# Performance work log

Measured on AMD Instinct MI355X. Metric: run time of the kernel, lower is better.

Reference implementation:

```python
import jax, jax.numpy as jnp
import numpy as np

N, E = 30000, 240000          # nodes, edges per view
IN, D, OUT = 512, 128, 64      # in_dim, hidden_dim, out_dim
V, BLK, H, DM = 2, 2, 2, 64    # num_view, blk_size, num_heads, gate max-pool dim
NEG_ATT, NEG_OUT = 0.2, 0.01   # leaky_relu slopes (attention / outer)


def setup_inputs() -> dict:
    key = jax.random.key(0)
    ks = jax.random.split(key, 12)
    s = 0.05
    f32 = jnp.float32
    return {
        "ft": jax.random.normal(ks[0], (N, IN), f32),
        "src": jax.random.randint(ks[1], (V, E), 0, N, jnp.int32),
        "dst": jax.random.randint(ks[2], (V, E), 0, N, jnp.int32),
        "W_proj": jax.random.normal(ks[3], (IN, D), f32) * s,
        "W_embed": jax.random.normal(ks[4], (D, D), f32) * s,
        "a_l": jax.random.normal(ks[5], (V, BLK, H, D), f32) * s,
        "a_r": jax.random.normal(ks[6], (V, BLK, H, D), f32) * s,
        "Wv": jax.random.normal(ks[7], (V, BLK, H, D, D), f32) * s,
        "Wgm": jax.random.normal(ks[8], (V, BLK, D, DM), f32) * s,
        "Wgate": jax.random.normal(ks[9], (V, BLK, 2 * D + DM, H), f32) * s,
        "b_gate": jnp.zeros((V, BLK, H), f32),
        "W_tran": jax.random.normal(ks[10], (2 * D + DM and (D + V * H * D), OUT), f32) * s if False else jax.random.normal(ks[10], (D + V * H * D, OUT), f32) * s,
        "b_tran": jnp.zeros((OUT,), f32),
    }


def _seg_sum(x, idx):
    return jax.ops.segment_sum(x, idx, num_segments=N)


def _cgaan_layer(v, z, s_idx, d_idx, al, ar, wv, wgm, wgate, bg, merge):
    # v: [N,D] values, z: [N,D] attention features ('proj_z')
    # Multi-head attention logits: e_ij = leaky_relu(a_l.z_src + a_r.z_dst)  [E,H]
    logit_l = jnp.einsum("nd,hd->nh", z, al)
    logit_r = jnp.einsum("nd,hd->nh", z, ar)
    e = jax.nn.leaky_relu(logit_l[s_idx] + logit_r[d_idx], NEG_ATT)
    # edge softmax over incoming edges of each dst node
    m = jax.ops.segment_max(e, d_idx, num_segments=N)          # [N,H]
    ex = jnp.exp(e - m[d_idx])
    denom = _seg_sum(ex, d_idx)                                 # [N,H]
    alpha = ex / denom[d_idx]                                   # [E,H]
    # per-head value projection and weighted aggregation
    wvn = jnp.einsum("nd,hde->nhe", v, wv)                      # [N,H,D]
    agg = _seg_sum(alpha[:, :, None] * wvn[s_idx], d_idx)       # [N,H,D]
    # GaAN-style gate: sigmoid(FC([x_i, mean_j v_j, max_j (v_j Wgm)])) -> per-head scalar
    deg = _seg_sum(jnp.ones((s_idx.shape[0],), v.dtype), d_idx)  # [N]
    mean_n = _seg_sum(v[s_idx], d_idx) / jnp.maximum(deg, 1.0)[:, None]
    mx = jax.ops.segment_max((v @ wgm)[s_idx], d_idx, num_segments=N)
    mx = jnp.where(deg[:, None] > 0, mx, 0.0)                   # isolated nodes -> 0
    g = jax.nn.sigmoid(jnp.concatenate([v, mean_n, mx], -1) @ wgate + bg)  # [N,H]
    agg = g[:, :, None] * agg
    if merge == "mean":
        return agg.mean(axis=1)                                 # [N,D]
    return agg.reshape(agg.shape[0], -1)                        # cat -> [N,H*D]


def reference(ft, src, dst, W_proj, W_embed, a_l, a_r, Wv, Wgm, Wgate, b_gate, W_tran, b_tran):
    proj = ft @ W_proj                                          # [N,D]
    cur = [proj for _ in range(V)]
    for i in range(BLK):
        merge = "mean" if i < BLK - 1 else "cat"
        nxt = []
        for j in range(V):
            z = cur[j] @ W_embed
            h = _cgaan_layer(cur[j], z, src[j], dst[j], a_l[j, i], a_r[j, i],
                             Wv[j, i], Wgm[j, i], Wgate[j, i], b_gate[j, i], merge)
            nxt.append(jax.nn.leaky_relu(h, NEG_OUT))
        cur = nxt
    h = jnp.concatenate([proj] + cur, axis=-1)                  # [N, D+V*H*D]
    return h @ W_tran + b_tran
```

## Files before the change

### kernel.cpp

```cpp
#include <hip/hip_runtime.h>
#include <hip/hip_bf16.h>
#include <math.h>

#define NN 30000
#define EE 240000
#define IN_DIM 512
#define DD 128
#define OUTD 64
#define NV 2
#define NBLK 2
#define NH 2
#define DMM 64
#define NEG_ATT 0.2f
#define NEG_OUT 0.01f
#define CH 1024
#define NCH ((NN + CH - 1) / CH)

typedef __attribute__((ext_vector_type(8))) short bf16x8;
typedef __attribute__((ext_vector_type(4))) float f32x4;
typedef __attribute__((ext_vector_type(4))) unsigned short us4;
typedef __attribute__((ext_vector_type(8))) unsigned short us8;

#define OFF_PROJVM 0
#define OFF_WV     131072
#define OFF_WGM    262144
#define OFF_TRAN   278528
#define WT_TOTAL   319488

__device__ __forceinline__ unsigned split_bf(float x) {
  unsigned u = __float_as_uint(x);
  unsigned hb = (u + 0x7FFFu + ((u >> 16) & 1u)) >> 16;
  float hf = __uint_as_float(hb << 16);
  float lo = x - hf;
  unsigned ul = __float_as_uint(lo);
  unsigned lb = (ul + 0x7FFFu + ((ul >> 16) & 1u)) >> 16;
  return hb | (lb << 16);
}

__device__ __forceinline__ unsigned short f2bf(float x) {
  unsigned u = __float_as_uint(x);
  return (unsigned short)((u + 0x7FFFu + ((u >> 16) & 1u)) >> 16);
}
__device__ __forceinline__ float bf2f(unsigned short u) {
  return __uint_as_float((unsigned)u << 16);
}

__device__ __forceinline__ void gload16(void* lds, const void* g) {
  __builtin_amdgcn_global_load_lds((const __attribute__((address_space(1))) unsigned int*)g,
                                   (__attribute__((address_space(3))) unsigned int*)lds, 16, 0, 0);
}

__global__ __launch_bounds__(256) void k_deg(const int* __restrict__ dst, int* __restrict__ deg) {
  int e = blockIdx.x * 256 + threadIdx.x;
  if (e < NV * EE) atomicAdd(&deg[(e / EE) * NN + dst[e]], 1);
}

__global__ __launch_bounds__(256) void k_scan1(const int* __restrict__ deg, int* __restrict__ partial) {
  int b = blockIdx.x, view = b / NCH, ch = b % NCH;
  const int* d = deg + view * NN + ch * CH;
  int rem = min(CH, NN - ch * CH);
  int t = threadIdx.x;
  int s = 0;
  for (int i = t; i < rem; i += 256) s += d[i];
  for (int k = 32; k; k >>= 1) s += __shfl_xor(s, k);
  __shared__ int wsum[4];
  if ((t & 63) == 0) wsum[t >> 6] = s;
  __syncthreads();
  if (t == 0) partial[b] = wsum[0] + wsum[1] + wsum[2] + wsum[3];
}

__global__ void k_scan2(const int* __restrict__ partial, int* __restrict__ chunkoff, int* __restrict__ off) {
  if (threadIdx.x == 0 && blockIdx.x == 0) {
    for (int v = 0; v < NV; v++) {
      int acc = 0;
      for (int c = 0; c < NCH; c++) { chunkoff[v * NCH + c] = acc; acc += partial[v * NCH + c]; }
      off[v * (NN + 1) + NN] = acc;
    }
  }
}

__global__ __launch_bounds__(256) void k_scan3(const int* __restrict__ deg, const int* __restrict__ chunkoff,
                                               int* __restrict__ off) {
  int b = blockIdx.x, view = b / NCH, ch = b % NCH;
  int base = ch * CH;
  const int* d = deg + view * NN;
  int* o = off + view * (NN + 1);
  int t = threadIdx.x, lane = t & 63, w = t >> 6;
  int i0 = base + t * 4;
  int x0 = 0, x1 = 0, x2 = 0, x3 = 0;
  if (i0 + 3 < NN) { int4 q = *(const int4*)(d + i0); x0 = q.x; x1 = q.y; x2 = q.z; x3 = q.w; }
  else {
    if (i0     < NN) x0 = d[i0];
    if (i0 + 1 < NN) x1 = d[i0 + 1];
    if (i0 + 2 < NN) x2 = d[i0 + 2];
  }
  int tot = x0 + x1 + x2 + x3;
  int incl = tot;
  for (int k = 1; k < 64; k <<= 1) { int y = __shfl_up(incl, k); if (lane >= k) incl += y; }
  __shared__ int wt[4];
  if (lane == 63) wt[w] = incl;
  __syncthreads();
  int wexcl = 0;
  for (int k = 0; k < w; k++) wexcl += wt[k];
  int excl = chunkoff[b] + wexcl + incl - tot;
  if (i0     < NN) o[i0]     = excl;
  if (i0 + 1 < NN) o[i0 + 1] = excl + x0;
  if (i0 + 2 < NN) o[i0 + 2] = excl + x0 + x1;
  if (i0 + 3 < NN) o[i0 + 3] = excl + x0 + x1 + x2;
}

__global__ __launch_bounds__(256) void k_fill(const int* __restrict__ src, const int* __restrict__ dst,
                                              const int* __restrict__ off, int* __restrict__ cursor,
                                              int* __restrict__ csr_src) {
  int e = blockIdx.x * 256 + threadIdx.x;
  if (e >= NV * EE) return;
  int view = e / EE;
  int d = dst[e];
  int p = atomicAdd(&cursor[view * NN + d], 1);
  csr_src[view * EE + off[view * (NN + 1) + d] + p] = src[e];
}

__global__ __launch_bounds__(256) void k_prep(const float* __restrict__ W_embed, const float* __restrict__ a_l,
                                              const float* __restrict__ a_r, float* __restrict__ Bl,
                                              float* __restrict__ Br) {
  int idx = blockIdx.x * 256 + threadIdx.x;
  if (idx >= NV * NBLK * DD * NH) return;
  int h = idx & 1, dd = (idx >> 1) & 127, lv = idx >> 8;
  const float* w = W_embed + dd * DD;
  const float* al = a_l + (lv * NH + h) * DD;
  const float* ar = a_r + (lv * NH + h) * DD;
  float sl = 0.f, sr = 0.f;
  for (int e = 0; e < DD; e++) { float we = w[e]; sl += we * al[e]; sr += we * ar[e]; }
  Bl[idx] = sl; Br[idx] = sr;
}

__global__ __launch_bounds__(256) void k_prep2(const float* __restrict__ Wp, const float* __restrict__ Wgm,
                                               float* __restrict__ wf) {
  int idx = blockIdx.x * 256 + threadIdx.x;
  int j = idx >> 15, k = (idx >> 6) & 511, n = idx & 63;
  const float* wp = Wp + (size_t)k * DD;
  const float* wg = Wgm + (size_t)(j * NBLK + 0) * DD * DMM + n;
  float s = 0.f;
  for (int e = 0; e < DD; e++) s += wp[e] * wg[(size_t)e * DMM];
  wf[idx] = s;
}

__global__ __launch_bounds__(256) void k_wsplit(const float* __restrict__ Wp, const float* __restrict__ wf,
                                                const float* __restrict__ Wv, const float* __restrict__ Wgm,
                                                const float* __restrict__ Wt,
                                                unsigned short* __restrict__ hi, unsigned short* __restrict__ lo) {
  int y = blockIdx.y;
  const float* src; int K, N; size_t doff;
  if (y == 0)      { src = Wp;                      K = 512; N = 128; doff = OFF_PROJVM; }
  else if (y <= 2) { int j = y - 1; src = wf + (size_t)j * 512 * 64; K = 512; N = 64; doff = OFF_PROJVM + (size_t)(128 + j * 64) * 512; }
  else if (y <= 6) { int lv = y - 3; src = Wv + (size_t)lv * 32768;  K = 256; N = 128; doff = OFF_WV + (size_t)lv * 32768; }
  else if (y <= 8) { int j = y - 7; src = Wgm + (size_t)(j * NBLK + 1) * 8192; K = 128; N = 64; doff = OFF_WGM + (size_t)j * 8192; }
  else             { src = Wt;                      K = 640; N = 64;  doff = OFF_TRAN; }
  int idx = blockIdx.x * 256 + threadIdx.x;
  if (idx >= K * N) return;
  int n = idx / K, k = idx % K;
  int tk = k >> 6, g = (k >> 3) & 7, j2 = k & 7;
  int ks = (tk << 6) | ((g ^ (n & 7)) << 3) | j2;
  unsigned p = split_bf(src[(size_t)k * N + n]);
  hi[doff + (size_t)n * K + ks] = (unsigned short)(p & 0xFFFFu);
  lo[doff + (size_t)n * K + ks] = (unsigned short)(p >> 16);
}

__global__ __launch_bounds__(256) void k_llr(const unsigned short* __restrict__ p0,
                                             const unsigned short* __restrict__ p1, int ps,
                                             const float* __restrict__ Bl0, const float* __restrict__ Br0,
                                             const float* __restrict__ Bl1, const float* __restrict__ Br1,
                                             float* __restrict__ ll, float* __restrict__ lr) {
  int lane = threadIdx.x & 63, wid = threadIdx.x >> 6;
  int n = blockIdx.x * 4 + wid;
  int k = lane * 2;
  unsigned a = *(const unsigned*)(p0 + (size_t)n * ps + k);
  unsigned b = *(const unsigned*)(p1 + (size_t)n * ps + k);
  float ax = bf2f((unsigned short)a), ay = bf2f((unsigned short)(a >> 16));
  float bx = bf2f((unsigned short)b), by = bf2f((unsigned short)(b >> 16));
  float r[8];
  r[0] = ax * Bl0[k * 2]     + ay * Bl0[k * 2 + 2];
  r[1] = ax * Bl0[k * 2 + 1] + ay * Bl0[k * 2 + 3];
  r[2] = ax * Br0[k * 2]     + ay * Br0[k * 2 + 2];
  r[3] = ax * Br0[k * 2 + 1] + ay * Br0[k * 2 + 3];
  r[4] = bx * Bl1[k * 2]     + by * Bl1[k * 2 + 2];
  r[5] = bx * Bl1[k * 2 + 1] + by * Bl1[k * 2 + 3];
  r[6] = bx * Br1[k * 2]     + by * Br1[k * 2 + 2];
  r[7] = bx * Br1[k * 2 + 1] + by * Br1[k * 2 + 3];
  for (int s = 32; s; s >>= 1)
#pragma unroll
    for (int q = 0; q < 8; q++) r[q] += __shfl_xor(r[q], s);
  if (lane == 0) {
    ll[n * 2] = r[0]; ll[n * 2 + 1] = r[1];
    lr[n * 2] = r[2]; lr[n * 2 + 1] = r[3];
    ll[NN * 2 + n * 2] = r[4]; ll[NN * 2 + n * 2 + 1] = r[5];
    lr[NN * 2 + n * 2] = r[6]; lr[NN * 2 + n * 2 + 1] = r[7];
  }
}

__global__ __launch_bounds__(256) void k_edge(const int* __restrict__ off_, const int* __restrict__ csr_,
                                              const float* __restrict__ ll_, const float* __restrict__ lr_,
                                              const unsigned short* __restrict__ pk_, long viewStride,
                                              int ps, int vmoff0, int vmstep,
                                              const float* __restrict__ Wg_, const float* __restrict__ bg_,
                                              unsigned short* __restrict__ S_) {
  int view = blockIdx.y;
  const int* off = off_ + view * (NN + 1);
  const int* csr = csr_ + (size_t)view * EE;
  const float* ll = ll_ + (size_t)view * NN * 2;
  const float* lr = lr_ + (size_t)view * NN * 2;
  const unsigned short* pk = pk_ + (size_t)view * viewStride;
  int vmoff = vmoff0 + view * vmstep;
  const float* Wg = Wg_ + (size_t)view * NBLK * (2 * DD + DMM) * NH;
  const float* bg = bg_ + view * NBLK * NH;
  unsigned short* S = S_ + (size_t)view * NN * 256;

  int lane = threadIdx.x & 63, wid = threadIdx.x >> 6;
  int n = blockIdx.x * 4 + wid;
  int e0 = off[n], nb = off[n + 1] - e0;
  int half = lane >> 5, hl = lane & 31;
  if (nb == 0) {
    us4 z4 = {0, 0, 0, 0};
    *(us4*)(S + (size_t)n * 256 + half * 128 + 4 * hl) = z4;
    return;
  }
  float lr0 = lr[n * 2], lr1 = lr[n * 2 + 1];
  float sa0[4] = {0.f, 0.f, 0.f, 0.f}, sa1[4] = {0.f, 0.f, 0.f, 0.f}, vs[4] = {0.f, 0.f, 0.f, 0.f};
  float d0 = 0.f, d1 = 0.f, vm0 = -INFINITY, vm1 = -INFINITY;
  for (int base = 0; base < nb; base += 64) {
    int i = base + lane;
    float w0 = 0.f, w1 = 0.f, fv = 0.f; int sidx = 0;
    if (i < nb) {
      sidx = csr[e0 + i];
      float x0 = ll[sidx * 2] + lr0, x1 = ll[sidx * 2 + 1] + lr1;
      x0 = (x0 > 0.f) ? x0 : NEG_ATT * x0;
      x1 = (x1 > 0.f) ? x1 : NEG_ATT * x1;
      w0 = __expf(x0); w1 = __expf(x1); fv = 1.f;
    }
    d0 += w0; d1 += w1;
    int cnt = min(64, nb - base);
    for (int s = 0; 2 * s < cnt; s++) {
      int j = 2 * s + half;
      int se = __shfl(sidx, j);
      float we0 = __shfl(w0, j), we1 = __shfl(w1, j), fe = __shfl(fv, j);
      if (fe != 0.f) {
        const unsigned short* rowp = pk + (size_t)se * ps;
        us4 vq = *(const us4*)(rowp + 4 * hl);
        float v0 = bf2f(vq[0]), v1 = bf2f(vq[1]), v2 = bf2f(vq[2]), v3 = bf2f(vq[3]);
        sa0[0] += we0 * v0; sa0[1] += we0 * v1; sa0[2] += we0 * v2; sa0[3] += we0 * v3;
        sa1[0] += we1 * v0; sa1[1] += we1 * v1; sa1[2] += we1 * v2; sa1[3] += we1 * v3;
        vs[0] += v0; vs[1] += v1; vs[2] += v2; vs[3] += v3;
        unsigned vmu = *(const unsigned*)(rowp + vmoff + 2 * hl);
        vm0 = fmaxf(vm0, bf2f((unsigned short)vmu));
        vm1 = fmaxf(vm1, bf2f((unsigned short)(vmu >> 16)));
      }
    }
  }
#pragma unroll
  for (int k = 0; k < 4; k++) {
    sa0[k] += __shfl_xor(sa0[k], 32);
    sa1[k] += __shfl_xor(sa1[k], 32);
    vs[k]  += __shfl_xor(vs[k], 32);
  }
  vm0 = fmaxf(vm0, __shfl_xor(vm0, 32));
  vm1 = fmaxf(vm1, __shfl_xor(vm1, 32));
  for (int s = 32; s; s >>= 1) { d0 += __shfl_xor(d0, s); d1 += __shfl_xor(d1, s); }
  unsigned vnu = *(const unsigned*)(pk + (size_t)n * ps + 2 * lane);
  float vnx = bf2f((unsigned short)vnu), vny = bf2f((unsigned short)(vnu >> 16));
  float im = 1.f / (float)nb;
  float p0 = vnx * Wg[(2 * lane) * 2]     + vny * Wg[(2 * lane + 1) * 2];
  float p1 = vnx * Wg[(2 * lane) * 2 + 1] + vny * Wg[(2 * lane + 1) * 2 + 1];
  if (half == 0) {
#pragma unroll
    for (int k = 0; k < 4; k++) {
      float mk = vs[k] * im;
      p0 += mk * Wg[(128 + 4 * hl + k) * 2];
      p1 += mk * Wg[(128 + 4 * hl + k) * 2 + 1];
    }
  } else {
    p0 += vm0 * Wg[(256 + 2 * hl) * 2]     + vm1 * Wg[(256 + 2 * hl + 1) * 2];
    p1 += vm0 * Wg[(256 + 2 * hl) * 2 + 1] + vm1 * Wg[(256 + 2 * hl + 1) * 2 + 1];
  }
  for (int s = 32; s; s >>= 1) { p0 += __shfl_xor(p0, s); p1 += __shfl_xor(p1, s); }
  float g0 = 1.f / (1.f + __expf(-(p0 + bg[0])));
  float g1 = 1.f / (1.f + __expf(-(p1 + bg[1])));
  float q0 = g0 / d0, q1 = g1 / d1;
  us4 o4;
  if (half == 0) {
    o4[0] = f2bf(sa0[0] * q0); o4[1] = f2bf(sa0[1] * q0);
    o4[2] = f2bf(sa0[2] * q0); o4[3] = f2bf(sa0[3] * q0);
  } else {
    o4[0] = f2bf(sa1[0] * q1); o4[1] = f2bf(sa1[1] * q1);
    o4[2] = f2bf(sa1[2] * q1); o4[3] = f2bf(sa1[3] * q1);
  }
  *(us4*)(S + (size_t)n * 256 + half * 128 + 4 * hl) = o4;
}

struct GB {
  const void* A[4];
  unsigned long long bofs[4];
  float* C[4];
  unsigned short* P[4];
  int ldc[4];
  int pldc[4];
};

template <int BN, bool ABF>
__global__ __launch_bounds__(256) void gemm_mfma(
    GB gb, const unsigned short* __restrict__ Bth, const unsigned short* __restrict__ Btl,
    int lda, int ldb, int M, int K,
    const float* __restrict__ bias, float fs, int flags) {
  constexpr int NSUB = BN / 32;
  constexpr int CPW = BN / 32;
  __shared__ __align__(16) unsigned short Ah[64][64];
  __shared__ __align__(16) unsigned short Al[ABF ? 2 : 64][64];
  __shared__ __align__(16) unsigned short Bh[BN][64], Bl[BN][64];
  const int z = blockIdx.z;
  const float* __restrict__ Af = (const float*)gb.A[z];
  const unsigned short* __restrict__ Ab = (const unsigned short*)gb.A[z];
  float* __restrict__ C = gb.C[z];
  unsigned short* __restrict__ P = gb.P[z];
  const int ldc = gb.ldc[z], pldc = gb.pldc[z];
  const size_t bofs = gb.bofs[z];
  const int t = threadIdx.x;
  const int lane = t & 63, wv = t >> 6;
  const int lm = lane & 15, lg = lane >> 4;
  const int m0w = (wv & 1) * 32, n0w = (wv >> 1) * (BN / 2);
  const int row0 = blockIdx.x * 64;
  f32x4 acc[2][NSUB];
#pragma unroll
  for (int ms = 0; ms < 2; ms++)
#pragma unroll
    for (int ns = 0; ns < NSUB; ns++) acc[ms][ns] = (f32x4)0.f;

  float4 apre[2][2];
  const int ar_ = t >> 3, ag_ = t & 7;

  auto loadA = [&](int k0) {
    if constexpr (!ABF) {
#pragma unroll
      for (int q = 0; q < 2; q++) {
        int rr = row0 + q * 32 + ar_;
        if (rr < M) {
          const float* p = Af + (size_t)rr * lda + k0 + ag_ * 8;
          apre[q][0] = *(const float4*)p;
          apre[q][1] = *(const float4*)(p + 4);
        } else {
          apre[q][0] = make_float4(0.f, 0.f, 0.f, 0.f);
          apre[q][1] = make_float4(0.f, 0.f, 0.f, 0.f);
        }
      }
    }
  };
  auto storeA = [&]() {
    if constexpr (!ABF) {
#pragma unroll
      for (int q = 0; q < 2; q++) {
        int r = q * 32 + ar_;
        us8 h8, l8;
        float vals[8] = {apre[q][0].x, apre[q][0].y, apre[q][0].z, apre[q][0].w,
                         apre[q][1].x, apre[q][1].y, apre[q][1].z, apre[q][1].w};
#pragma unroll
        for (int e = 0; e < 8; e++) {
          unsigned pp = split_bf(vals[e]);
          h8[e] = (unsigned short)(pp & 0xFFFFu);
          l8[e] = (unsigned short)(pp >> 16);
        }
        int c = (ag_ ^ (r & 7)) << 3;
        *(us8*)&Ah[r][c] = h8;
        *(us8*)&Al[r][c] = l8;
      }
    }
  };
  auto stageA_bf = [&](int k0) {
    if constexpr (ABF) {
#pragma unroll
      for (int q = 0; q < 2; q++) {
        int r = q * 32 + ar_;
        int rr = min(row0 + r, M - 1);
        int scg = ag_ ^ (r & 7);
        gload16((char*)&Ah[0][0] + q * 4096 + t * 16,
                Ab + (size_t)rr * lda + k0 + scg * 8);
      }
    }
  };
  auto stageB = [&](int k0) {
#pragma unroll
    for (int q = 0; q < CPW; q++) {
      int chunk = wv * CPW + q;
      int o = chunk * 1024 + lane * 16;
      int n = o >> 7;
      int pq = (o >> 4) & 7;
      size_t gofs = bofs + (size_t)n * ldb + k0 + pq * 8;
      gload16((char*)&Bh[0][0] + o, Bth + gofs);
      gload16((char*)&Bl[0][0] + o, Btl + gofs);
    }
  };

  loadA(0);
  for (int k0 = 0; k0 < K; k0 += 64) {
    if constexpr (ABF) stageA_bf(k0); else storeA();
    stageB(k0);
    __syncthreads();
    if constexpr (!ABF) { if (k0 + 64 < K) loadA(k0 + 64); }
#pragma unroll
    for (int kc = 0; kc < 2; kc++) {
      bf16x8 afh[2], afl[2], bfh[NSUB], bfl[NSUB];
#pragma unroll
      for (int ms = 0; ms < 2; ms++) {
        int R = m0w + ms * 16 + lm;
        int c = (((kc * 4 + lg) ^ (R & 7)) << 3);
        afh[ms] = *(const bf16x8*)&Ah[R][c];
        if constexpr (!ABF) afl[ms] = *(const bf16x8*)&Al[R][c];
      }
#pragma unroll
      for (int ns = 0; ns < NSUB; ns++) {
        int R = n0w + ns * 16 + lm;
        int c = (((kc * 4 + lg) ^ (R & 7)) << 3);
        bfh[ns] = *(const bf16x8*)&Bh[R][c];
        bfl[ns] = *(const bf16x8*)&Bl[R][c];
      }
#pragma unroll
      for (int ms = 0; ms < 2; ms++)
#pragma unroll
        for (int ns = 0; ns < NSUB; ns++) {
          if constexpr (!ABF)
            acc[ms][ns] = __builtin_amdgcn_mfma_f32_16x16x32_bf16(afl[ms], bfh[ns], acc[ms][ns], 0, 0, 0);
          acc[ms][ns] = __builtin_amdgcn_mfma_f32_16x16x32_bf16(afh[ms], bfl[ns], acc[ms][ns], 0, 0, 0);
          acc[ms][ns] = __builtin_amdgcn_mfma_f32_16x16x32_bf16(afh[ms], bfh[ns], acc[ms][ns], 0, 0, 0);
        }
    }
    __syncthreads();
  }
#pragma unroll
  for (int ms = 0; ms < 2; ms++)
#pragma unroll
    for (int ns = 0; ns < NSUB; ns++)
#pragma unroll
      for (int j = 0; j < 4; j++) {
        int row = row0 + m0w + ms * 16 + lg * 4 + j;
        if (row >= M) continue;
        int col = n0w + ns * 16 + lm;
        float val = acc[ms][ns][j] * fs;
        if (bias) val += bias[col];
        if (flags & 2) val = (val > 0.f) ? val : NEG_OUT * val;
        if (C) C[(size_t)row * ldc + col] = val;
        if (P) P[(size_t)row * pldc + col] = f2bf(val);
      }
}

extern "C" void kernel_launch(void* const* d_in, const int* in_sizes, int n_in,
                              void* d_out, int out_size, void* d_ws, size_t ws_size,
                              hipStream_t stream) {
  const float* ft      = (const float*)d_in[0];
  const int*   src     = (const int*)  d_in[1];
  const int*   dst     = (const int*)  d_in[2];
  const float* W_proj  = (const float*)d_in[3];
  const float* W_embed = (const float*)d_in[4];
  const float* a_l     = (const float*)d_in[5];
  const float* a_r     = (const float*)d_in[6];
  const float* Wv      = (const float*)d_in[7];
  const float* Wgm     = (const float*)d_in[8];
  const float* Wgate   = (const float*)d_in[9];
  const float* b_gate  = (const float*)d_in[10];
  const float* W_tran  = (const float*)d_in[11];
  const float* b_tran  = (const float*)d_in[12];
  float* out = (float*)d_out;
  char* ws = (char*)d_ws;
  (void)in_sizes; (void)n_in; (void)out_size; (void)ws_size;

  size_t o = 0;
  auto take = [&](size_t bytes) { size_t r = o; o += (bytes + 255) & ~(size_t)255; return r; };
  int*   deg     = (int*)(ws + take((size_t)NV * NN * 4));
  int*   cursor  = (int*)(ws + take((size_t)NV * NN * 4));
  int*   csr_off = (int*)(ws + take((size_t)NV * (NN + 1) * 4));
  int*   csr_src = (int*)(ws + take((size_t)NV * EE * 4));
  int*   partial = (int*)(ws + take((size_t)NV * NCH * 4));
  int*   chunkoff= (int*)(ws + take((size_t)NV * NCH * 4));
  float* Bl      = (float*)(ws + take((size_t)NV * NBLK * DD * NH * 4));
  float* Br      = (float*)(ws + take((size_t)NV * NBLK * DD * NH * 4));
  float* wf      = (float*)(ws + take((size_t)NV * 512 * 64 * 4));
  unsigned short* whi = (unsigned short*)(ws + take((size_t)WT_TOTAL * 2));
  unsigned short* wlo = (unsigned short*)(ws + take((size_t)WT_TOTAL * 2));
  float* h       = (float*)(ws + take((size_t)NN * 640 * 4));
  unsigned short* pk0 = (unsigned short*)(ws + take((size_t)NN * 256 * 2));
  unsigned short* pk1 = (unsigned short*)(ws + take((size_t)NV * NN * 192 * 2));
  unsigned short* Sbf = (unsigned short*)(ws + take((size_t)NV * NN * 256 * 2));
  float* llb     = (float*)(ws + take((size_t)NV * NN * NH * 4));
  float* lrb     = (float*)(ws + take((size_t)NV * NN * NH * 4));

  const int HSTR = 640;

  hipMemsetAsync(deg, 0, (size_t)(((size_t)NV * NN * 4 + 255) & ~(size_t)255) + (size_t)NV * NN * 4, stream);
  k_deg<<<(NV * EE + 255) / 256, 256, 0, stream>>>(dst, deg);
  k_scan1<<<NV * NCH, 256, 0, stream>>>(deg, partial);
  k_scan2<<<1, 64, 0, stream>>>(partial, chunkoff, csr_off);
  k_scan3<<<NV * NCH, 256, 0, stream>>>(deg, chunkoff, csr_off);
  k_fill<<<(NV * EE + 255) / 256, 256, 0, stream>>>(src, dst, csr_off, cursor, csr_src);
  k_prep<<<(NV * NBLK * DD * NH + 255) / 256, 256, 0, stream>>>(W_embed, a_l, a_r, Bl, Br);
  k_prep2<<<256, 256, 0, stream>>>(W_proj, Wgm, wf);
  k_wsplit<<<dim3(256, 10), 256, 0, stream>>>(W_proj, wf, Wv, Wgm, W_tran, whi, wlo);

  const int GM = (NN + 63) / 64;

  {
    GB gb = {};
    gb.A[0] = ft; gb.A[1] = ft;
    gb.bofs[0] = OFF_PROJVM; gb.bofs[1] = OFF_PROJVM + (size_t)128 * 512;
    gb.C[0] = h;  gb.ldc[0] = HSTR;
    gb.P[0] = pk0;       gb.pldc[0] = 256;
    gb.P[1] = pk0 + 128; gb.pldc[1] = 256;
    gemm_mfma<128, false><<<dim3(GM, 1, 2), 256, 0, stream>>>(gb, whi, wlo, IN_DIM, 512, NN, 512,
                                                              nullptr, 1.f, 0);
  }

  k_llr<<<NN / 4, 256, 0, stream>>>(pk0, pk0, 256,
                                    Bl + 0 * 256, Br + 0 * 256, Bl + 2 * 256, Br + 2 * 256, llb, lrb);
  k_edge<<<dim3(NN / 4, 2), 256, 0, stream>>>(csr_off, csr_src, llb, lrb,
                                              pk0, 0L, 256, 128, 64,
                                              Wgate, b_gate, Sbf);
  {
    GB gb = {};
    for (int j = 0; j < 2; j++) {
      gb.A[j] = Sbf + (size_t)j * NN * 256;
      gb.bofs[j] = OFF_WV + (size_t)(j * 2) * 32768;
      gb.P[j] = pk1 + (size_t)j * NN * 192;
      gb.pldc[j] = 192;
    }
    gemm_mfma<128, true><<<dim3(GM, 1, 2), 256, 0, stream>>>(gb, whi, wlo, 256, 256, NN, 256,
                                                             nullptr, 0.5f, 2);
  }
  {
    GB gb = {};
    for (int j = 0; j < 2; j++) {
      gb.A[j] = pk1 + (size_t)j * NN * 192;
      gb.bofs[j] = OFF_WGM + (size_t)j * 8192;
      gb.P[j] = pk1 + (size_t)j * NN * 192 + 128;
      gb.pldc[j] = 192;
    }
    gemm_mfma<64, true><<<dim3(GM, 1, 2), 256, 0, stream>>>(gb, whi, wlo, 192, 128, NN, 128,
                                                            nullptr, 1.f, 0);
  }
  k_llr<<<NN / 4, 256, 0, stream>>>(pk1, pk1 + (size_t)NN * 192, 192,
                                    Bl + 1 * 256, Br + 1 * 256, Bl + 3 * 256, Br + 3 * 256, llb, lrb);
  k_edge<<<dim3(NN / 4, 2), 256, 0, stream>>>(csr_off, csr_src, llb, lrb,
                                              pk1, (long)NN * 192, 192, 128, 0,
                                              Wgate + (size_t)(2 * DD + DMM) * NH, b_gate + NH, Sbf);
  {
    GB gb = {};
    for (int z = 0; z < 4; z++) {
      int j = z >> 1, hd = z & 1;
      gb.A[z] = Sbf + (size_t)j * NN * 256 + hd * 128;
      gb.bofs[z] = OFF_WV + (size_t)(j * 2 + 1) * 32768 + hd * 128;
      gb.C[z] = h + 128 + z * 128;
      gb.ldc[z] = HSTR;
    }
    gemm_mfma<128, true><<<dim3(GM, 1, 4), 256, 0, stream>>>(gb, whi, wlo, 256, 256, NN, 128,
                                                             nullptr, 1.f, 2);
  }
  {
    GB gb = {};
    gb.A[0] = h; gb.bofs[0] = OFF_TRAN; gb.C[0] = out; gb.ldc[0] = OUTD;
    gemm_mfma<64, false><<<dim3(GM, 1, 1), 256, 0, stream>>>(gb, whi, wlo, HSTR, 640, NN, 640,
                                                             b_tran, 1.f, 0);
  }
}
```

Before: 328.6 us.

## Precompute per-node gate mean projections and fold into edge logit loads

The gate's neighbour-mean term is moved out of the edge loop. Each node's value projection onto the mean-part gate weights is precomputed in k_llr and packed with the left logits into a float4. The edge kernel then sums two scalars per edge instead of accumulating a 128-wide value sum and reducing it across lanes. The two weight-prep kernels are also merged into one launch, and the first GEMM's z-dimension is folded into the x grid. The cost is extra reductions in k_llr and wider per-node records.

```diff
diff --git a/kernel.cpp b/kernel.cpp
--- a/kernel.cpp
+++ b/kernel.cpp
@@ -120,29 +120,30 @@
   csr_src[view * EE + off[view * (NN + 1) + d] + p] = src[e];
 }
 
-__global__ __launch_bounds__(256) void k_prep(const float* __restrict__ W_embed, const float* __restrict__ a_l,
-                                              const float* __restrict__ a_r, float* __restrict__ Bl,
-                                              float* __restrict__ Br) {
-  int idx = blockIdx.x * 256 + threadIdx.x;
-  if (idx >= NV * NBLK * DD * NH) return;
-  int h = idx & 1, dd = (idx >> 1) & 127, lv = idx >> 8;
-  const float* w = W_embed + dd * DD;
-  const float* al = a_l + (lv * NH + h) * DD;
-  const float* ar = a_r + (lv * NH + h) * DD;
-  float sl = 0.f, sr = 0.f;
-  for (int e = 0; e < DD; e++) { float we = w[e]; sl += we * al[e]; sr += we * ar[e]; }
-  Bl[idx] = sl; Br[idx] = sr;
-}
-
-__global__ __launch_bounds__(256) void k_prep2(const float* __restrict__ Wp, const float* __restrict__ Wgm,
+__global__ __launch_bounds__(256) void k_prepw(const float* __restrict__ W_embed, const float* __restrict__ a_l,
+                                               const float* __restrict__ a_r, const float* __restrict__ Wp,
+                                               const float* __restrict__ Wgm,
+                                               float* __restrict__ Bl, float* __restrict__ Br,
                                                float* __restrict__ wf) {
-  int idx = blockIdx.x * 256 + threadIdx.x;
-  int j = idx >> 15, k = (idx >> 6) & 511, n = idx & 63;
-  const float* wp = Wp + (size_t)k * DD;
-  const float* wg = Wgm + (size_t)(j * NBLK + 0) * DD * DMM + n;
-  float s = 0.f;
-  for (int e = 0; e < DD; e++) s += wp[e] * wg[(size_t)e * DMM];
-  wf[idx] = s;
+  if (blockIdx.x < 256) {
+    int idx = blockIdx.x * 256 + threadIdx.x;
+    int j = idx >> 15, k = (idx >> 6) & 511, n = idx & 63;
+    const float* wp = Wp + (size_t)k * DD;
+    const float* wg = Wgm + (size_t)(j * NBLK + 0) * DD * DMM + n;
+    float s = 0.f;
+    for (int e = 0; e < DD; e++) s += wp[e] * wg[(size_t)e * DMM];
+    wf[idx] = s;
+  } else {
+    int idx = (blockIdx.x - 256) * 256 + threadIdx.x;
+    if (idx >= NV * NBLK * DD * NH) return;
+    int h = idx & 1, dd = (idx >> 1) & 127, lv = idx >> 8;
+    const float* w = W_embed + dd * DD;
+    const float* al = a_l + (lv * NH + h) * DD;
+    const float* ar = a_r + (lv * NH + h) * DD;
+    float sl = 0.f, sr = 0.f;
+    for (int e = 0; e < DD; e++) { float we = w[e]; sl += we * al[e]; sr += we * ar[e]; }
+    Bl[idx] = sl; Br[idx] = sr;
+  }
 }
 
 __global__ __launch_bounds__(256) void k_wsplit(const float* __restrict__ Wp, const float* __restrict__ wf,
@@ -170,7 +171,8 @@
                                              const unsigned short* __restrict__ p1, int ps,
                                              const float* __restrict__ Bl0, const float* __restrict__ Br0,
                                              const float* __restrict__ Bl1, const float* __restrict__ Br1,
-                                             float* __restrict__ ll, float* __restrict__ lr) {
+                                             const float* __restrict__ Wg0, const float* __restrict__ Wg1,
+                                             float4* __restrict__ lq, float2* __restrict__ lr) {
   int lane = threadIdx.x & 63, wid = threadIdx.x >> 6;
   int n = blockIdx.x * 4 + wid;
   int k = lane * 2;
@@ -178,28 +180,32 @@
   unsigned b = *(const unsigned*)(p1 + (size_t)n * ps + k);
   float ax = bf2f((unsigned short)a), ay = bf2f((unsigned short)(a >> 16));
   float bx = bf2f((unsigned short)b), by = bf2f((unsigned short)(b >> 16));
-  float r[8];
-  r[0] = ax * Bl0[k * 2]     + ay * Bl0[k * 2 + 2];
-  r[1] = ax * Bl0[k * 2 + 1] + ay * Bl0[k * 2 + 3];
-  r[2] = ax * Br0[k * 2]     + ay * Br0[k * 2 + 2];
-  r[3] = ax * Br0[k * 2 + 1] + ay * Br0[k * 2 + 3];
-  r[4] = bx * Bl1[k * 2]     + by * Bl1[k * 2 + 2];
-  r[5] = bx * Bl1[k * 2 + 1] + by * Bl1[k * 2 + 3];
-  r[6] = bx * Br1[k * 2]     + by * Br1[k * 2 + 2];
-  r[7] = bx * Br1[k * 2 + 1] + by * Br1[k * 2 + 3];
+  float r[12];
+  r[0]  = ax * Bl0[k * 2]     + ay * Bl0[k * 2 + 2];
+  r[1]  = ax * Bl0[k * 2 + 1] + ay * Bl0[k * 2 + 3];
+  r[2]  = ax * Br0[k * 2]     + ay * Br0[k * 2 + 2];
+  r[3]  = ax * Br0[k * 2 + 1] + ay * Br0[k * 2 + 3];
+  r[4]  = ax * Wg0[(128 + k) * 2]     + ay * Wg0[(129 + k) * 2];
+  r[5]  = ax * Wg0[(128 + k) * 2 + 1] + ay * Wg0[(129 + k) * 2 + 1];
+  r[6]  = bx * Bl1[k * 2]     + by * Bl1[k * 2 + 2];
+  r[7]  = bx * Bl1[k * 2 + 1] + by * Bl1[k * 2 + 3];
+  r[8]  = bx * Br1[k * 2]     + by * Br1[k * 2 + 2];
+  r[9]  = bx * Br1[k * 2 + 1] + by * Br1[k * 2 + 3];
+  r[10] = bx * Wg1[(128 + k) * 2]     + by * Wg1[(129 + k) * 2];
+  r[11] = bx * Wg1[(128 + k) * 2 + 1] + by * Wg1[(129 + k) * 2 + 1];
   for (int s = 32; s; s >>= 1)
 #pragma unroll
-    for (int q = 0; q < 8; q++) r[q] += __shfl_xor(r[q], s);
+    for (int q = 0; q < 12; q++) r[q] += __shfl_xor(r[q], s);
   if (lane == 0) {
-    ll[n * 2] = r[0]; ll[n * 2 + 1] = r[1];
-    lr[n * 2] = r[2]; lr[n * 2 + 1] = r[3];
-    ll[NN * 2 + n * 2] = r[4]; ll[NN * 2 + n * 2 + 1] = r[5];
-    lr[NN * 2 + n * 2] = r[6]; lr[NN * 2 + n * 2 + 1] = r[7];
+    lq[n] = make_float4(r[0], r[1], r[4], r[5]);
+    lr[n] = make_float2(r[2], r[3]);
+    lq[NN + n] = make_float4(r[6], r[7], r[10], r[11]);
+    lr[NN + n] = make_float2(r[8], r[9]);
   }
 }
 
 __global__ __launch_bounds__(256) void k_edge(const int* __restrict__ off_, const int* __restrict__ csr_,
-                                              const float* __restrict__ ll_, const float* __restrict__ lr_,
+                                              const float4* __restrict__ lq_, const float2* __restrict__ lr_,
                                               const unsigned short* __restrict__ pk_, long viewStride,
                                               int ps, int vmoff0, int vmstep,
                                               const float* __restrict__ Wg_, const float* __restrict__ bg_,
@@ -207,8 +213,8 @@
   int view = blockIdx.y;
   const int* off = off_ + view * (NN + 1);
   const int* csr = csr_ + (size_t)view * EE;
-  const float* ll = ll_ + (size_t)view * NN * 2;
-  const float* lr = lr_ + (size_t)view * NN * 2;
+  const float4* lq = lq_ + (size_t)view * NN;
+  const float2* lrp = lr_ + (size_t)view * NN;
   const unsigned short* pk = pk_ + (size_t)view * viewStride;
   int vmoff = vmoff0 + view * vmstep;
   const float* Wg = Wg_ + (size_t)view * NBLK * (2 * DD + DMM) * NH;
@@ -224,32 +230,32 @@
     *(us4*)(S + (size_t)n * 256 + half * 128 + 4 * hl) = z4;
     return;
   }
-  float lr0 = lr[n * 2], lr1 = lr[n * 2 + 1];
-  float sa0[4] = {0.f, 0.f, 0.f, 0.f}, sa1[4] = {0.f, 0.f, 0.f, 0.f}, vs[4] = {0.f, 0.f, 0.f, 0.f};
-  float d0 = 0.f, d1 = 0.f, vm0 = -INFINITY, vm1 = -INFINITY;
+  float2 lrn = lrp[n];
+  float sa0[4] = {0.f, 0.f, 0.f, 0.f}, sa1[4] = {0.f, 0.f, 0.f, 0.f};
+  float d0 = 0.f, d1 = 0.f, tm0 = 0.f, tm1 = 0.f, vm0 = -INFINITY, vm1 = -INFINITY;
   for (int base = 0; base < nb; base += 64) {
     int i = base + lane;
-    float w0 = 0.f, w1 = 0.f, fv = 0.f; int sidx = 0;
+    float w0 = 0.f, w1 = 0.f; int sidx = 0;
     if (i < nb) {
       sidx = csr[e0 + i];
-      float x0 = ll[sidx * 2] + lr0, x1 = ll[sidx * 2 + 1] + lr1;
+      float4 q = lq[sidx];
+      float x0 = q.x + lrn.x, x1 = q.y + lrn.y;
       x0 = (x0 > 0.f) ? x0 : NEG_ATT * x0;
       x1 = (x1 > 0.f) ? x1 : NEG_ATT * x1;
-      w0 = __expf(x0); w1 = __expf(x1); fv = 1.f;
-    }
-    d0 += w0; d1 += w1;
+      w0 = __expf(x0); w1 = __expf(x1);
+      d0 += w0; d1 += w1; tm0 += q.z; tm1 += q.w;
+    }
     int cnt = min(64, nb - base);
     for (int s = 0; 2 * s < cnt; s++) {
       int j = 2 * s + half;
-      int se = __shfl(sidx, j);
-      float we0 = __shfl(w0, j), we1 = __shfl(w1, j), fe = __shfl(fv, j);
-      if (fe != 0.f) {
+      if (j < cnt) {
+        int se = __shfl(sidx, j);
+        float we0 = __shfl(w0, j), we1 = __shfl(w1, j);
         const unsigned short* rowp = pk + (size_t)se * ps;
         us4 vq = *(const us4*)(rowp + 4 * hl);
         float v0 = bf2f(vq[0]), v1 = bf2f(vq[1]), v2 = bf2f(vq[2]), v3 = bf2f(vq[3]);
         sa0[0] += we0 * v0; sa0[1] += we0 * v1; sa0[2] += we0 * v2; sa0[3] += we0 * v3;
         sa1[0] += we1 * v0; sa1[1] += we1 * v1; sa1[2] += we1 * v2; sa1[3] += we1 * v3;
-        vs[0] += v0; vs[1] += v1; vs[2] += v2; vs[3] += v3;
         unsigned vmu = *(const unsigned*)(rowp + vmoff + 2 * hl);
         vm0 = fmaxf(vm0, bf2f((unsigned short)vmu));
         vm1 = fmaxf(vm1, bf2f((unsigned short)(vmu >> 16)));
@@ -260,7 +266,6 @@
   for (int k = 0; k < 4; k++) {
     sa0[k] += __shfl_xor(sa0[k], 32);
     sa1[k] += __shfl_xor(sa1[k], 32);
-    vs[k]  += __shfl_xor(vs[k], 32);
   }
   vm0 = fmaxf(vm0, __shfl_xor(vm0, 32));
   vm1 = fmaxf(vm1, __shfl_xor(vm1, 32));
@@ -268,16 +273,9 @@
   unsigned vnu = *(const unsigned*)(pk + (size_t)n * ps + 2 * lane);
   float vnx = bf2f((unsigned short)vnu), vny = bf2f((unsigned short)(vnu >> 16));
   float im = 1.f / (float)nb;
-  float p0 = vnx * Wg[(2 * lane) * 2]     + vny * Wg[(2 * lane + 1) * 2];
-  float p1 = vnx * Wg[(2 * lane) * 2 + 1] + vny * Wg[(2 * lane + 1) * 2 + 1];
-  if (half == 0) {
-#pragma unroll
-    for (int k = 0; k < 4; k++) {
-      float mk = vs[k] * im;
-      p0 += mk * Wg[(128 + 4 * hl + k) * 2];
-      p1 += mk * Wg[(128 + 4 * hl + k) * 2 + 1];
-    }
-  } else {
+  float p0 = vnx * Wg[(2 * lane) * 2]     + vny * Wg[(2 * lane + 1) * 2]     + tm0 * im;
+  float p1 = vnx * Wg[(2 * lane) * 2 + 1] + vny * Wg[(2 * lane + 1) * 2 + 1] + tm1 * im;
+  if (half == 1) {
     p0 += vm0 * Wg[(256 + 2 * hl) * 2]     + vm1 * Wg[(256 + 2 * hl + 1) * 2];
     p1 += vm0 * Wg[(256 + 2 * hl) * 2 + 1] + vm1 * Wg[(256 + 2 * hl + 1) * 2 + 1];
   }
@@ -315,7 +313,9 @@
   __shared__ __align__(16) unsigned short Ah[64][64];
   __shared__ __align__(16) unsigned short Al[ABF ? 2 : 64][64];
   __shared__ __align__(16) unsigned short Bh[BN][64], Bl[BN][64];
-  const int z = blockIdx.z;
+  int z, xb;
+  if (flags & 4) { z = blockIdx.x & 1; xb = blockIdx.x >> 1; }
+  else           { z = blockIdx.z;     xb = blockIdx.x; }
   const float* __restrict__ Af = (const float*)gb.A[z];
   const unsigned short* __restrict__ Ab = (const unsigned short*)gb.A[z];
   float* __restrict__ C = gb.C[z];
@@ -326,7 +326,7 @@
   const int lane = t & 63, wv = t >> 6;
   const int lm = lane & 15, lg = lane >> 4;
   const int m0w = (wv & 1) * 32, n0w = (wv >> 1) * (BN / 2);
-  const int row0 = blockIdx.x * 64;
+  const int row0 = xb * 64;
   f32x4 acc[2][NSUB];
 #pragma unroll
   for (int ms = 0; ms < 2; ms++)
@@ -486,8 +486,8 @@
   unsigned short* pk0 = (unsigned short*)(ws + take((size_t)NN * 256 * 2));
   unsigned short* pk1 = (unsigned short*)(ws + take((size_t)NV * NN * 192 * 2));
   unsigned short* Sbf = (unsigned short*)(ws + take((size_t)NV * NN * 256 * 2));
-  float* llb     = (float*)(ws + take((size_t)NV * NN * NH * 4));
-  float* lrb     = (float*)(ws + take((size_t)NV * NN * NH * 4));
+  float4* lqb    = (float4*)(ws + take((size_t)NV * NN * 16));
+  float2* lrb    = (float2*)(ws + take((size_t)NV * NN * 8));
 
   const int HSTR = 640;
 
@@ -497,8 +497,7 @@
   k_scan2<<<1, 64, 0, stream>>>(partial, chunkoff, csr_off);
   k_scan3<<<NV * NCH, 256, 0, stream>>>(deg, chunkoff, csr_off);
   k_fill<<<(NV * EE + 255) / 256, 256, 0, stream>>>(src, dst, csr_off, cursor, csr_src);
-  k_prep<<<(NV * NBLK * DD * NH + 255) / 256, 256, 0, stream>>>(W_embed, a_l, a_r, Bl, Br);
-  k_prep2<<<256, 256, 0, stream>>>(W_proj, Wgm, wf);
+  k_prepw<<<260, 256, 0, stream>>>(W_embed, a_l, a_r, W_proj, Wgm, Bl, Br, wf);
   k_wsplit<<<dim3(256, 10), 256, 0, stream>>>(W_proj, wf, Wv, Wgm, W_tran, whi, wlo);
 
   const int GM = (NN + 63) / 64;
@@ -510,13 +509,15 @@
     gb.C[0] = h;  gb.ldc[0] = HSTR;
     gb.P[0] = pk0;       gb.pldc[0] = 256;
     gb.P[1] = pk0 + 128; gb.pldc[1] = 256;
-    gemm_mfma<128, false><<<dim3(GM, 1, 2), 256, 0, stream>>>(gb, whi, wlo, IN_DIM, 512, NN, 512,
-                                                              nullptr, 1.f, 0);
+    gemm_mfma<128, false><<<dim3(GM * 2, 1, 1), 256, 0, stream>>>(gb, whi, wlo, IN_DIM, 512, NN, 512,
+                                                                  nullptr, 1.f, 4);
   }
 
   k_llr<<<NN / 4, 256, 0, stream>>>(pk0, pk0, 256,
-                                    Bl + 0 * 256, Br + 0 * 256, Bl + 2 * 256, Br + 2 * 256, llb, lrb);
-  k_edge<<<dim3(NN / 4, 2), 256, 0, stream>>>(csr_off, csr_src, llb, lrb,
+                                    Bl + 0 * 256, Br + 0 * 256, Bl + 2 * 256, Br + 2 * 256,
+                                    Wgate, Wgate + (size_t)NBLK * 320 * NH,
+                                    lqb, lrb);
+  k_edge<<<dim3(NN / 4, 2), 256, 0, stream>>>(csr_off, csr_src, lqb, lrb,
                                               pk0, 0L, 256, 128, 64,
                                               Wgate, b_gate, Sbf);
   {
@@ -542,10 +543,12 @@
                                                             nullptr, 1.f, 0);
   }
   k_llr<<<NN / 4, 256, 0, stream>>>(pk1, pk1 + (size_t)NN * 192, 192,
-                                    Bl + 1 * 256, Br + 1 * 256, Bl + 3 * 256, Br + 3 * 256, llb, lrb);
-  k_edge<<<dim3(NN / 4, 2), 256, 0, stream>>>(csr_off, csr_src, llb, lrb,
+                                    Bl + 1 * 256, Br + 1 * 256, Bl + 3 * 256, Br + 3 * 256,
+                                    Wgate + 640, Wgate + (size_t)NBLK * 640 + 640,
+                                    lqb, lrb);
+  k_edge<<<dim3(NN / 4, 2), 256, 0, stream>>>(csr_off, csr_src, lqb, lrb,
                                               pk1, (long)NN * 192, 192, 128, 0,
-                                              Wgate + (size_t)(2 * DD + DMM) * NH, b_gate + NH, Sbf);
+                                              Wgate + 640, b_gate + NH, Sbf);
   {
     GB gb = {};
     for (int z = 0; z < 4; z++) {
```

Result: no change. 334.7 us (+1.9%).
